# Kernel optimization log

Hardware: AMD Instinct MI355X
Metric: run time of the kernel (lower is better)

The kernel has to match this reference:

```python
import jax, jax.numpy as jnp
import numpy as np

D_MODEL, N_HEADS, D_LATENT = 1024, 16, 256
HEAD_DIM = D_MODEL // N_HEADS
B, T = 2, 2048


def apply_rope(x):
    # x: [B, T, H, D]
    Tn, D = x.shape[1], x.shape[3]
    inv_freq = 1.0 / (10000.0 ** (jnp.arange(0, D, 2, dtype=jnp.float32) / D))
    t = jnp.arange(Tn, dtype=jnp.float32)
    freqs = jnp.outer(t, inv_freq)               # [T, D/2]
    sin_f = jnp.sin(freqs)[None, :, None, :]
    cos_f = jnp.cos(freqs)[None, :, None, :]
    x1, x2 = jnp.split(x, 2, axis=-1)
    return jnp.concatenate([x1 * cos_f - x2 * sin_f,
                            x1 * sin_f + x2 * cos_f], axis=-1)


def setup_inputs() -> dict:
    key = jax.random.key(0)
    ks = jax.random.split(key, 5)
    s = lambda fan_in: 1.0 / np.sqrt(fan_in)
    return {
        "x": jax.random.normal(ks[0], (B, T, D_MODEL), jnp.float32),
        "Wq": jax.random.normal(ks[1], (D_MODEL, D_MODEL), jnp.float32) * s(D_MODEL),
        "bq": jnp.zeros((D_MODEL,), jnp.float32),
        "Wkv_down": jax.random.normal(ks[2], (D_MODEL, D_LATENT), jnp.float32) * s(D_MODEL),
        "bkv_down": jnp.zeros((D_LATENT,), jnp.float32),
        "Wkv_up": jax.random.normal(ks[3], (D_LATENT, 2 * D_MODEL), jnp.float32) * s(D_LATENT),
        "bkv_up": jnp.zeros((2 * D_MODEL,), jnp.float32),
        "Wo": jax.random.normal(ks[4], (D_MODEL, D_MODEL), jnp.float32) * s(D_MODEL),
        "bo": jnp.zeros((D_MODEL,), jnp.float32),
    }


def reference(x, Wq, bq, Wkv_down, bkv_down, Wkv_up, bkv_up, Wo, bo):
    Bn, Tn = x.shape[0], x.shape[1]
    q = x @ Wq + bq                              # [B, T, d_model]
    kv = (x @ Wkv_down + bkv_down) @ Wkv_up + bkv_up  # [B, T, 2*d_model]
    q = q.reshape(Bn, Tn, N_HEADS, HEAD_DIM)
    kv = kv.reshape(Bn, Tn, N_HEADS, 2 * HEAD_DIM)
    k, v = jnp.split(kv, 2, axis=-1)
    q = apply_rope(q)
    k = apply_rope(k)
    q = q.transpose(0, 2, 1, 3)                  # [B, H, T, D]
    k = k.transpose(0, 2, 1, 3)
    v = v.transpose(0, 2, 1, 3)

    att = jnp.einsum('bhqd,bhkd->bhqk', q, k) / jnp.sqrt(jnp.float32(HEAD_DIM))

    idx = jnp.arange(Tn, dtype=jnp.float32)
    dist_signed = idx[:, None] - idx[None, :]    # [T, T]
    log_sparse = -0.1 * jnp.log(jnp.abs(dist_signed) + 1.0)
    decay = jnp.exp(-jnp.maximum(dist_signed, 0.0) * 0.01)
    att = att + (log_sparse + jnp.log(decay + 1e-9))[None, None]
    att = jax.nn.softmax(att, axis=-1)
    out = jnp.einsum('bhqk,bhkd->bhqd', att, v)  # [B, H, T, D]

    # Infini/memory branch: mean-pooled single-slot attention
    memory_k = jnp.mean(k, axis=2, keepdims=True)  # [B, H, 1, D]
    memory_v = jnp.mean(v, axis=2, keepdims=True)
    memory_scores = jnp.einsum('bhqd,bhkd->bhqk', q, memory_k)  # [B, H, T, 1]
    infini_out = jax.nn.sigmoid(memory_scores) * memory_v       # [B, H, T, D]
    out = out + 0.2 * infini_out

    out = out.transpose(0, 2, 1, 3).reshape(Bn, Tn, D_MODEL)
    return out @ Wo + bo
```

## Files before the change

kernel.cpp:

```cpp
#include <hip/hip_runtime.h>
#include <hip/hip_bf16.h>

#define D_MODEL 1024
#define N_HEADS 16
#define HEAD_DIM 64
#define D_LATENT 256
#define BATCH 2
#define SEQ 2048
#define M_ROWS (BATCH * SEQ)

typedef __bf16 bf16;
typedef __attribute__((ext_vector_type(4))) __bf16 bf16x4;
typedef __attribute__((ext_vector_type(8))) __bf16 bf16x8;
typedef __attribute__((ext_vector_type(4))) float f32x4;

#define MFMA_BF16(a, b, c) __builtin_amdgcn_mfma_f32_16x16x32_bf16((a), (b), (c), 0, 0, 0)
#define LOG2E 1.4426950408889634f

__device__ __forceinline__ void gll16(const void* g, void* l) {
    __builtin_amdgcn_global_load_lds(
        (const __attribute__((address_space(1))) unsigned int*)g,
        (__attribute__((address_space(3))) unsigned int*)l, 16, 0, 0);
}

__device__ __forceinline__ void tw_body(
    const float* __restrict__ W, bf16* __restrict__ Wt, int K, int N,
    int b, float (*tw)[33], int tid)
{
    int nx = N / 32;
    int n0 = (b % nx) * 32, k0 = (b / nx) * 32;
    int c = tid & 31, r = tid >> 5;
    #pragma unroll
    for (int it = 0; it < 4; ++it)
        tw[r + it * 8][c] = W[(size_t)(k0 + r + it * 8) * N + n0 + c];
    __syncthreads();
    #pragma unroll
    for (int it = 0; it < 4; ++it)
        Wt[(size_t)(n0 + r + it * 8) * K + k0 + c] = (bf16)tw[c][r + it * 8];
}

__global__ __launch_bounds__(256) void prep_all(
    const float* __restrict__ x, bf16* __restrict__ xb,
    const float* __restrict__ Wq, bf16* __restrict__ Wqt,
    const float* __restrict__ Wd, bf16* __restrict__ Wdt,
    const float* __restrict__ Wu, bf16* __restrict__ Wut,
    const float* __restrict__ Wo, bf16* __restrict__ Wot,
    float2* __restrict__ rtab, float* __restrict__ bias2)
{
    __shared__ float tw[32][33];
    const int bid = blockIdx.x, tid = threadIdx.x;
    if (bid < 2048) {
        int i = bid * 256 + tid;
        const float4* s = ((const float4*)x) + (size_t)i * 2;
        float4 a = s[0], b = s[1];
        bf16x8 v;
        v[0] = (bf16)a.x; v[1] = (bf16)a.y; v[2] = (bf16)a.z; v[3] = (bf16)a.w;
        v[4] = (bf16)b.x; v[5] = (bf16)b.y; v[6] = (bf16)b.z; v[7] = (bf16)b.w;
        *(bf16x8*)(xb + (size_t)i * 8) = v;
    } else if (bid < 3072) {
        tw_body(Wq, Wqt, 1024, 1024, bid - 2048, tw, tid);
    } else if (bid < 3328) {
        tw_body(Wd, Wdt, 1024, 256, bid - 3072, tw, tid);
    } else if (bid < 3840) {
        tw_body(Wu, Wut, 256, 2048, bid - 3328, tw, tid);
    } else if (bid < 4864) {
        tw_body(Wo, Wot, 1024, 1024, bid - 3840, tw, tid);
    } else if (bid < 5120) {
        int i = (bid - 4864) * 256 + tid;
        int j = i & 31, t = i >> 5;
        float inv_freq = exp2f((float)j * -0.4152410118609203f);
        float ang = (float)t * inv_freq;
        float sn, cs; sincosf(ang, &sn, &cs);
        rtab[i] = make_float2(cs, sn);
    } else {
        int i = (bid - 5120) * 256 + tid;
        if (i < 2 * SEQ - 1) {
            float d = (float)(i - (SEQ - 1));
            float ls  = -0.1f * logf(fabsf(d) + 1.0f);
            float dec = expf(-fmaxf(d, 0.0f) * 0.01f);
            bias2[i] = (ls + logf(dec + 1e-9f)) * LOG2E;
        }
    }
}

__device__ __forceinline__ void gemm_body(
    const bf16* __restrict__ A, const bf16* __restrict__ Bt, int K,
    bf16* As, bf16* Bs, f32x4 (&acc)[4][4],
    int m0, int n0, int tid, int l15, int lh, int wr, int wc)
{
    for (int k0 = 0; k0 < K; k0 += 32) {
        __syncthreads();
        #pragma unroll
        for (int it = 0; it < 2; ++it) {
            int c = it * 256 + tid;
            int row = c >> 2, part = c & 3;
            int p = part ^ ((row >> 1) & 3);
            gll16(A  + (size_t)(m0 + row) * K + k0 + p * 8, As + c * 8);
            gll16(Bt + (size_t)(n0 + row) * K + k0 + p * 8, Bs + c * 8);
        }
        __syncthreads();
        bf16x8 af[4], bg[4];
        #pragma unroll
        for (int i = 0; i < 4; ++i) {
            int row = wr * 64 + i * 16 + l15;
            int cc = lh ^ ((row >> 1) & 3);
            af[i] = *(const bf16x8*)(As + row * 32 + cc * 8);
        }
        #pragma unroll
        for (int j = 0; j < 4; ++j) {
            int row = wc * 64 + j * 16 + l15;
            int cc = lh ^ ((row >> 1) & 3);
            bg[j] = *(const bf16x8*)(Bs + row * 32 + cc * 8);
        }
        #pragma unroll
        for (int i = 0; i < 4; ++i)
            #pragma unroll
            for (int j = 0; j < 4; ++j)
                acc[i][j] = MFMA_BF16(af[i], bg[j], acc[i][j]);
    }
}

template<int OUT_BF16>
__global__ __launch_bounds__(256) void gemm_plain(
    const bf16* __restrict__ A, const bf16* __restrict__ Bt,
    const float* __restrict__ bias, void* __restrict__ C,
    int N, int K)
{
    __shared__ bf16 As[128 * 32];
    __shared__ bf16 Bs[128 * 32];
    const int tid = threadIdx.x, lane = tid & 63, w = tid >> 6;
    const int wr = w >> 1, wc = w & 1;
    const int l15 = lane & 15, lh = lane >> 4;
    const int m0 = blockIdx.y * 128, n0 = blockIdx.x * 128;
    f32x4 acc[4][4] = {};
    gemm_body(A, Bt, K, As, Bs, acc, m0, n0, tid, l15, lh, wr, wc);

    #pragma unroll
    for (int i = 0; i < 4; ++i) {
        int row = m0 + wr * 64 + i * 16 + lh * 4;
        #pragma unroll
        for (int j = 0; j < 4; ++j) {
            int col = n0 + wc * 64 + j * 16 + l15;
            float bv = bias[col];
            #pragma unroll
            for (int r = 0; r < 4; ++r) {
                float v = acc[i][j][r] + bv;
                if (OUT_BF16) ((bf16*)C)[(size_t)(row + r) * N + col] = (bf16)v;
                else          ((float*)C)[(size_t)(row + r) * N + col] = v;
            }
        }
    }
}

__global__ __launch_bounds__(256) void gemm_q_rope(
    const bf16* __restrict__ A, const bf16* __restrict__ Bt,
    const float* __restrict__ bias, const float2* __restrict__ rtab,
    bf16* __restrict__ Qh)
{
    __shared__ bf16 As[128 * 32];
    __shared__ bf16 Bs[128 * 32];
    const int tid = threadIdx.x, lane = tid & 63, w = tid >> 6;
    const int wr = w >> 1, wc = w & 1;
    const int l15 = lane & 15, lh = lane >> 4;
    const int m0 = blockIdx.y * 128, n0 = blockIdx.x * 128;
    f32x4 acc[4][4] = {};
    gemm_body(A, Bt, D_MODEL, As, Bs, acc, m0, n0, tid, l15, lh, wr, wc);

    const int head = blockIdx.x * 2 + wc;
    #pragma unroll
    for (int i = 0; i < 4; ++i) {
        #pragma unroll
        for (int r = 0; r < 4; ++r) {
            int m = m0 + wr * 64 + i * 16 + lh * 4 + r;
            int tpos = m & (SEQ - 1), b = m >> 11;
            bf16* orow = Qh + ((size_t)(b * N_HEADS + head) * SEQ + tpos) * 64;
            #pragma unroll
            for (int j01 = 0; j01 < 2; ++j01) {
                int jj = j01 * 16 + l15;
                float2 cssn = rtab[tpos * 32 + jj];
                float v1 = acc[i][j01][r]     + bias[head * 64 + jj];
                float v2 = acc[i][j01 + 2][r] + bias[head * 64 + jj + 32];
                orow[jj]      = (bf16)(v1 * cssn.x - v2 * cssn.y);
                orow[jj + 32] = (bf16)(v1 * cssn.y + v2 * cssn.x);
            }
        }
    }
}

__global__ __launch_bounds__(256) void gemm_kv_rope(
    const bf16* __restrict__ A, const bf16* __restrict__ Bt,
    const float* __restrict__ bias, const float2* __restrict__ rtab,
    bf16* __restrict__ Kh, bf16* __restrict__ Vh)
{
    __shared__ bf16 As[128 * 32];
    __shared__ bf16 Bs[128 * 32];
    const int tid = threadIdx.x, lane = tid & 63, w = tid >> 6;
    const int wr = w >> 1, wc = w & 1;
    const int l15 = lane & 15, lh = lane >> 4;
    const int m0 = blockIdx.y * 128, n0 = blockIdx.x * 128;
    f32x4 acc[4][4] = {};
    gemm_body(A, Bt, D_LATENT, As, Bs, acc, m0, n0, tid, l15, lh, wr, wc);

    const int head = blockIdx.x;
    if (wc == 0) {
        #pragma unroll
        for (int i = 0; i < 4; ++i) {
            #pragma unroll
            for (int r = 0; r < 4; ++r) {
                int m = m0 + wr * 64 + i * 16 + lh * 4 + r;
                int tpos = m & (SEQ - 1), b = m >> 11;
                bf16* orow = Kh + ((size_t)(b * N_HEADS + head) * SEQ + tpos) * 64;
                #pragma unroll
                for (int j01 = 0; j01 < 2; ++j01) {
                    int jj = j01 * 16 + l15;
                    float2 cssn = rtab[tpos * 32 + jj];
                    float v1 = acc[i][j01][r]     + bias[head * 128 + jj];
                    float v2 = acc[i][j01 + 2][r] + bias[head * 128 + jj + 32];
                    orow[jj]      = (bf16)(v1 * cssn.x - v2 * cssn.y);
                    orow[jj + 32] = (bf16)(v1 * cssn.y + v2 * cssn.x);
                }
            }
        }
    } else {
        #pragma unroll
        for (int i = 0; i < 4; ++i) {
            #pragma unroll
            for (int r = 0; r < 4; ++r) {
                int m = m0 + wr * 64 + i * 16 + lh * 4 + r;
                int tpos = m & (SEQ - 1), b = m >> 11;
                bf16* orow = Vh + ((size_t)(b * N_HEADS + head) * SEQ + tpos) * 64;
                #pragma unroll
                for (int j = 0; j < 4; ++j) {
                    int d = j * 16 + l15;
                    orow[d] = (bf16)(acc[i][j][r] + bias[head * 128 + 64 + d]);
                }
            }
        }
    }
}

__global__ __launch_bounds__(256) void transpose_v_b(
    const bf16* __restrict__ Vh, bf16* __restrict__ Vt)
{
    __shared__ bf16 tile[64][72];
    int blk = blockIdx.x;
    int tt = blk & 31, bh = blk >> 5;
    int t0 = tt * 64;
    int tid = threadIdx.x;
    #pragma unroll
    for (int it = 0; it < 2; ++it) {
        int lin = it * 256 + tid;
        int r = lin >> 3, c8 = (lin & 7) * 8;
        bf16x8 v = *(const bf16x8*)(Vh + ((size_t)bh * SEQ + t0 + r) * 64 + c8);
        #pragma unroll
        for (int e = 0; e < 8; ++e) tile[c8 + e][r] = v[e];
    }
    __syncthreads();
    #pragma unroll
    for (int it = 0; it < 2; ++it) {
        int lin = it * 256 + tid;
        int d = lin >> 3, seg = (lin & 7) * 8;
        bf16x8 v = *(const bf16x8*)(&tile[d][seg]);
        *(bf16x8*)(Vt + ((size_t)bh * 64 + d) * SEQ + t0 + seg) = v;
    }
}

__global__ __launch_bounds__(256) void mean_part(
    const bf16* __restrict__ Kh, const bf16* __restrict__ Vh,
    float* __restrict__ part)
{
    __shared__ float red[4][128];
    const int bh = blockIdx.x >> 3, seg = blockIdx.x & 7;
    const int tid = threadIdx.x;
    const int rr = tid >> 4, l16 = tid & 15;
    float ak[4] = {}, av[4] = {};
    #pragma unroll 4
    for (int i = 0; i < 16; ++i) {
        int row = seg * 256 + i * 16 + rr;
        const bf16* kp = Kh + ((size_t)bh * SEQ + row) * 64 + l16 * 4;
        const bf16* vp = Vh + ((size_t)bh * SEQ + row) * 64 + l16 * 4;
        bf16x4 k4 = *(const bf16x4*)kp;
        bf16x4 v4 = *(const bf16x4*)vp;
        #pragma unroll
        for (int e = 0; e < 4; ++e) { ak[e] += (float)k4[e]; av[e] += (float)v4[e]; }
    }
    #pragma unroll
    for (int m = 16; m <= 32; m <<= 1)
        #pragma unroll
        for (int e = 0; e < 4; ++e) {
            ak[e] += __shfl_xor(ak[e], m, 64);
            av[e] += __shfl_xor(av[e], m, 64);
        }
    int wv = tid >> 6;
    if ((tid & 63) < 16) {
        #pragma unroll
        for (int e = 0; e < 4; ++e) {
            red[wv][l16 * 4 + e]      = ak[e];
            red[wv][64 + l16 * 4 + e] = av[e];
        }
    }
    __syncthreads();
    if (tid < 128) {
        float s = red[0][tid] + red[1][tid] + red[2][tid] + red[3][tid];
        part[((size_t)seg * 32 + bh) * 128 + tid] = s;
    }
}

__global__ void mean_final(const float* __restrict__ part, float* __restrict__ memkv)
{
    int idx = blockIdx.x * 256 + threadIdx.x;
    float s = 0.f;
    #pragma unroll
    for (int g = 0; g < 8; ++g) s += part[(size_t)g * 4096 + idx];
    memkv[idx] = s * (1.f / SEQ);
}

__global__ __launch_bounds__(256) void attn_mfma(
    const bf16* __restrict__ Qh,
    const bf16* __restrict__ Kh,
    const bf16* __restrict__ Vt,
    const float* __restrict__ bias2,
    const float* __restrict__ memkv,
    bf16* __restrict__ ao)
{
    __shared__ bf16 PQ[4 * 16 * 88];
    __shared__ bf16 Ks[64 * 64];
    __shared__ bf16 Vs[64 * 64];
    __shared__ float bias_s[2112];

    const int tid = threadIdx.x;
    const int lane = tid & 63;
    const int w = tid >> 6;
    const int l15 = lane & 15, lh = lane >> 4;
    const int bh = blockIdx.y;
    const int q0 = blockIdx.x * 64;
    const size_t bhT = (size_t)bh * SEQ;

    for (int i = tid; i < 2111; i += 256) bias_s[i] = bias2[q0 + i];
    #pragma unroll
    for (int it = 0; it < 2; ++it) {
        int c = it * 256 + tid;
        int row = c >> 3, part = c & 7;
        int p = part ^ (row & 7);
        gll16(Qh + (bhT + q0 + row) * 64 + p * 8, PQ + c * 8);
    }
    __syncthreads();

    const int qrow = w * 16 + l15;
    bf16x8 qf[2];
    #pragma unroll
    for (int ks = 0; ks < 2; ++ks) {
        int pp = (ks * 4 + lh) ^ (qrow & 7);
        qf[ks] = *(const bf16x8*)(PQ + qrow * 64 + pp * 8);
    }

    const float* mk = memkv + bh * 128;
    float di = 0.f;
    #pragma unroll
    for (int ks = 0; ks < 2; ++ks)
        #pragma unroll
        for (int e = 0; e < 8; ++e)
            di += (float)qf[ks][e] * mk[ks * 32 + lh * 8 + e];
    di += __shfl_xor(di, 16, 64);
    di += __shfl_xor(di, 32, 64);

    f32x4 o[4] = {};
    float lsum = 0.f;
    bf16* Psw = PQ + w * 16 * 88;

    for (int kt = 0; kt < SEQ / 64; ++kt) {
        __syncthreads();
        #pragma unroll
        for (int it = 0; it < 2; ++it) {
            int c = it * 256 + tid;
            int row = c >> 3, part = c & 7;
            int p = part ^ (row & 7);
            gll16(Kh + (bhT + kt * 64 + row) * 64 + p * 8, Ks + c * 8);
            gll16(Vt + ((size_t)bh * 64 + row) * SEQ + kt * 64 + p * 8, Vs + c * 8);
        }
        __syncthreads();

        f32x4 s_[4] = {};
        #pragma unroll
        for (int ks = 0; ks < 2; ++ks) {
            #pragma unroll
            for (int jk = 0; jk < 4; ++jk) {
                int row = jk * 16 + l15;
                int cc = (ks * 4 + lh) ^ (row & 7);
                bf16x8 kf = *(const bf16x8*)(Ks + row * 64 + cc * 8);
                s_[jk] = MFMA_BF16(kf, qf[ks], s_[jk]);
            }
        }

        #pragma unroll
        for (int jk = 0; jk < 4; ++jk) {
            int idx0 = (w * 16 + l15) - (kt * 64 + jk * 16 + lh * 4) + 2047;
            bf16x4 pb;
            #pragma unroll
            for (int r = 0; r < 4; ++r) {
                float pexp = exp2f(s_[jk][r] * (0.125f * LOG2E) + bias_s[idx0 - r]);
                lsum += pexp;
                pb[r] = (bf16)pexp;
            }
            *(bf16x4*)(Psw + l15 * 88 + jk * 16 + lh * 4) = pb;
        }

        #pragma unroll
        for (int ks = 0; ks < 2; ++ks) {
            bf16x8 pf = *(const bf16x8*)(Psw + l15 * 88 + ks * 32 + lh * 8);
            #pragma unroll
            for (int jd = 0; jd < 4; ++jd) {
                int row = jd * 16 + l15;
                int cc = (ks * 4 + lh) ^ (row & 7);
                bf16x8 vf = *(const bf16x8*)(Vs + row * 64 + cc * 8);
                o[jd] = MFMA_BF16(pf, vf, o[jd]);
            }
        }
    }

    lsum += __shfl_xor(lsum, 16, 64);
    lsum += __shfl_xor(lsum, 32, 64);

    float inv_l[4], sig[4];
    #pragma unroll
    for (int r = 0; r < 4; ++r) {
        int src = lh * 4 + r;
        inv_l[r] = 1.f / __shfl(lsum, src, 64);
        float dd = __shfl(di, src, 64);
        sig[r] = 1.f / (1.f + __expf(-dd));
    }

    const int b = bh >> 4, h = bh & 15;
    #pragma unroll
    for (int jd = 0; jd < 4; ++jd) {
        int d = jd * 16 + l15;
        float mv = mk[64 + d];
        #pragma unroll
        for (int r = 0; r < 4; ++r) {
            int qi = q0 + w * 16 + lh * 4 + r;
            float val = o[jd][r] * inv_l[r] + 0.2f * sig[r] * mv;
            ao[((size_t)(b * SEQ + qi)) * D_MODEL + h * 64 + d] = (bf16)val;
        }
    }
}

extern "C" void kernel_launch(void* const* d_in, const int* in_sizes, int n_in,
                              void* d_out, int out_size, void* d_ws, size_t ws_size,
                              hipStream_t stream)
{
    const float* x        = (const float*)d_in[0];
    const float* Wq       = (const float*)d_in[1];
    const float* bq       = (const float*)d_in[2];
    const float* Wkv_down = (const float*)d_in[3];
    const float* bkv_down = (const float*)d_in[4];
    const float* Wkv_up   = (const float*)d_in[5];
    const float* bkv_up   = (const float*)d_in[6];
    const float* Wo       = (const float*)d_in[7];
    const float* bo       = (const float*)d_in[8];
    float* out = (float*)d_out;

    char* p = (char*)d_ws;
    bf16* xb   = (bf16*)p;  p += 8388608;
    bf16* Wqt  = (bf16*)p;  p += 2097152;
    bf16* Wdt  = (bf16*)p;  p += 524288;
    bf16* Wut  = (bf16*)p;  p += 1048576;
    bf16* Wot  = (bf16*)p;  p += 2097152;
    bf16* kvd  = (bf16*)p;  p += 2097152;
    bf16* Qh   = (bf16*)p;  p += 8388608;
    bf16* Kh   = (bf16*)p;  p += 8388608;
    bf16* Vh   = (bf16*)p;  p += 8388608;
    bf16* Vt   = (bf16*)p;  p += 8388608;
    bf16* ao   = (bf16*)p;  p += 8388608;
    float* memb  = (float*)p; p += 16384;
    float* bias2 = (float*)p; p += 16384;
    float2* rtab = (float2*)p; p += 524288;
    float* partb = (float*)p; p += 131072;

    dim3 blk(256);

    prep_all<<<dim3(5136), blk, 0, stream>>>(
        x, xb, Wq, Wqt, Wkv_down, Wdt, Wkv_up, Wut, Wo, Wot, rtab, bias2);

    gemm_plain<1><<<dim3(D_LATENT / 128, M_ROWS / 128), blk, 0, stream>>>(
        xb, Wdt, bkv_down, kvd, D_LATENT, D_MODEL);
    gemm_q_rope<<<dim3(D_MODEL / 128, M_ROWS / 128), blk, 0, stream>>>(
        xb, Wqt, bq, rtab, Qh);
    gemm_kv_rope<<<dim3(2 * D_MODEL / 128, M_ROWS / 128), blk, 0, stream>>>(
        kvd, Wut, bkv_up, rtab, Kh, Vh);

    transpose_v_b<<<dim3(BATCH * N_HEADS * (SEQ / 64)), blk, 0, stream>>>(Vh, Vt);
    mean_part<<<dim3(BATCH * N_HEADS * 8), blk, 0, stream>>>(Kh, Vh, partb);
    mean_final<<<dim3(16), blk, 0, stream>>>(partb, memb);

    attn_mfma<<<dim3(SEQ / 64, BATCH * N_HEADS), blk, 0, stream>>>(
        Qh, Kh, Vt, bias2, memb, ao);

    gemm_plain<0><<<dim3(D_MODEL / 128, M_ROWS / 128), blk, 0, stream>>>(
        ao, Wot, bo, out, D_MODEL, D_MODEL);
}
```

Baseline: 256.0 us.

## Double-buffer GEMM and attention tiles, fuse Q/KV-down GEMMs and V transpose/mean

GEMM and attention main loops now double-buffer their LDS tiles, prefetching the next K-slice with global_load_lds and waiting on a partial vmcnt before a single barrier. The Q-projection and KV-down GEMMs are merged into one launch. The KV-up GEMM epilogue writes V already transposed through LDS and accumulates the K/V means with atomics into a buffer zeroed in prep. Together these remove the separate transpose and mean kernels, several launches and a global V round trip, at the cost of doubled LDS per block and float atomic ordering nondeterminism in the means.

```diff
diff --git a/kernel.cpp b/kernel.cpp
--- a/kernel.cpp
+++ b/kernel.cpp
@@ -16,12 +16,16 @@
 
 #define MFMA_BF16(a, b, c) __builtin_amdgcn_mfma_f32_16x16x32_bf16((a), (b), (c), 0, 0, 0)
 #define LOG2E 1.4426950408889634f
+#define SBAR() __builtin_amdgcn_s_barrier()
+#define SCHED0() __builtin_amdgcn_sched_barrier(0)
 
 __device__ __forceinline__ void gll16(const void* g, void* l) {
     __builtin_amdgcn_global_load_lds(
         (const __attribute__((address_space(1))) unsigned int*)g,
         (__attribute__((address_space(3))) unsigned int*)l, 16, 0, 0);
 }
+__device__ __forceinline__ void vwait4() { asm volatile("s_waitcnt vmcnt(4)" ::: "memory"); }
+__device__ __forceinline__ void vwait0() { asm volatile("s_waitcnt vmcnt(0)" ::: "memory"); }
 
 __device__ __forceinline__ void tw_body(
     const float* __restrict__ W, bf16* __restrict__ Wt, int K, int N,
@@ -45,7 +49,8 @@
     const float* __restrict__ Wd, bf16* __restrict__ Wdt,
     const float* __restrict__ Wu, bf16* __restrict__ Wut,
     const float* __restrict__ Wo, bf16* __restrict__ Wot,
-    float2* __restrict__ rtab, float* __restrict__ bias2)
+    float2* __restrict__ rtab, float* __restrict__ bias2,
+    float* __restrict__ memb)
 {
     __shared__ float tw[32][33];
     const int bid = blockIdx.x, tid = threadIdx.x;
@@ -80,25 +85,42 @@
             float dec = expf(-fmaxf(d, 0.0f) * 0.01f);
             bias2[i] = (ls + logf(dec + 1e-9f)) * LOG2E;
         }
+        if (i < 4096) memb[i] = 0.f;
+    }
+}
+
+__device__ __forceinline__ void stage_gemm(
+    const bf16* __restrict__ A, const bf16* __restrict__ Bt, int K, int k0,
+    bf16* As, bf16* Bs, int m0, int n0, int tid)
+{
+    #pragma unroll
+    for (int it = 0; it < 2; ++it) {
+        int c = it * 256 + tid;
+        int row = c >> 2, part = c & 3;
+        int p = part ^ ((row >> 1) & 3);
+        gll16(A  + (size_t)(m0 + row) * K + k0 + p * 8, As + c * 8);
+        gll16(Bt + (size_t)(n0 + row) * K + k0 + p * 8, Bs + c * 8);
     }
 }
 
 __device__ __forceinline__ void gemm_body(
     const bf16* __restrict__ A, const bf16* __restrict__ Bt, int K,
-    bf16* As, bf16* Bs, f32x4 (&acc)[4][4],
+    bf16* sh, f32x4 (&acc)[4][4],
     int m0, int n0, int tid, int l15, int lh, int wr, int wc)
 {
+    stage_gemm(A, Bt, K, 0, sh, sh + 8192, m0, n0, tid);
+    int cur = 0;
     for (int k0 = 0; k0 < K; k0 += 32) {
-        __syncthreads();
-        #pragma unroll
-        for (int it = 0; it < 2; ++it) {
-            int c = it * 256 + tid;
-            int row = c >> 2, part = c & 3;
-            int p = part ^ ((row >> 1) & 3);
-            gll16(A  + (size_t)(m0 + row) * K + k0 + p * 8, As + c * 8);
-            gll16(Bt + (size_t)(n0 + row) * K + k0 + p * 8, Bs + c * 8);
-        }
-        __syncthreads();
+        if (k0 + 32 < K) {
+            stage_gemm(A, Bt, K, k0 + 32, sh + (cur ^ 1) * 4096,
+                       sh + 8192 + (cur ^ 1) * 4096, m0, n0, tid);
+            vwait4();
+        } else {
+            vwait0();
+        }
+        SCHED0(); SBAR(); SCHED0();
+        const bf16* As = sh + cur * 4096;
+        const bf16* Bs = sh + 8192 + cur * 4096;
         bf16x8 af[4], bg[4];
         #pragma unroll
         for (int i = 0; i < 4; ++i) {
@@ -117,23 +139,171 @@
             #pragma unroll
             for (int j = 0; j < 4; ++j)
                 acc[i][j] = MFMA_BF16(af[i], bg[j], acc[i][j]);
-    }
-}
-
-template<int OUT_BF16>
-__global__ __launch_bounds__(256) void gemm_plain(
+        SCHED0(); SBAR(); SCHED0();
+        cur ^= 1;
+    }
+}
+
+__global__ __launch_bounds__(256) void gemm_qkvd(
+    const bf16* __restrict__ xb,
+    const bf16* __restrict__ Wqt, const float* __restrict__ bq,
+    const float2* __restrict__ rtab, bf16* __restrict__ Qh,
+    const bf16* __restrict__ Wdt, const float* __restrict__ bkvd,
+    bf16* __restrict__ kvd)
+{
+    __shared__ bf16 sh[16384];
+    const int tid = threadIdx.x, lane = tid & 63, w = tid >> 6;
+    const int wr = w >> 1, wc = w & 1;
+    const int l15 = lane & 15, lh = lane >> 4;
+    const int bx = blockIdx.x;
+    const int m0 = blockIdx.y * 128;
+    const bf16* Bt = (bx < 8) ? Wqt : Wdt;
+    const int n0 = (bx < 8) ? bx * 128 : (bx - 8) * 128;
+
+    f32x4 acc[4][4] = {};
+    gemm_body(xb, Bt, D_MODEL, sh, acc, m0, n0, tid, l15, lh, wr, wc);
+
+    if (bx < 8) {
+        const int head = bx * 2 + wc;
+        #pragma unroll
+        for (int i = 0; i < 4; ++i) {
+            #pragma unroll
+            for (int r = 0; r < 4; ++r) {
+                int m = m0 + wr * 64 + i * 16 + lh * 4 + r;
+                int tpos = m & (SEQ - 1), b = m >> 11;
+                bf16* orow = Qh + ((size_t)(b * N_HEADS + head) * SEQ + tpos) * 64;
+                #pragma unroll
+                for (int j01 = 0; j01 < 2; ++j01) {
+                    int jj = j01 * 16 + l15;
+                    float2 cssn = rtab[tpos * 32 + jj];
+                    float v1 = acc[i][j01][r]     + bq[head * 64 + jj];
+                    float v2 = acc[i][j01 + 2][r] + bq[head * 64 + jj + 32];
+                    orow[jj]      = (bf16)(v1 * cssn.x - v2 * cssn.y);
+                    orow[jj + 32] = (bf16)(v1 * cssn.y + v2 * cssn.x);
+                }
+            }
+        }
+    } else {
+        #pragma unroll
+        for (int i = 0; i < 4; ++i) {
+            int row = m0 + wr * 64 + i * 16 + lh * 4;
+            #pragma unroll
+            for (int j = 0; j < 4; ++j) {
+                int col = n0 + wc * 64 + j * 16 + l15;
+                float bv = bkvd[col];
+                #pragma unroll
+                for (int r = 0; r < 4; ++r)
+                    kvd[(size_t)(row + r) * D_LATENT + col] = (bf16)(acc[i][j][r] + bv);
+            }
+        }
+    }
+}
+
+__global__ __launch_bounds__(256) void gemm_kv_rope(
     const bf16* __restrict__ A, const bf16* __restrict__ Bt,
-    const float* __restrict__ bias, void* __restrict__ C,
-    int N, int K)
-{
-    __shared__ bf16 As[128 * 32];
-    __shared__ bf16 Bs[128 * 32];
+    const float* __restrict__ bias, const float2* __restrict__ rtab,
+    bf16* __restrict__ Kh, bf16* __restrict__ Vt, float* __restrict__ memb)
+{
+    __shared__ bf16 sh[16384];
+    const int tid = threadIdx.x, lane = tid & 63, w = tid >> 6;
+    const int wr = w >> 1, wc = w & 1;
+    const int l15 = lane & 15, lh = lane >> 4;
+    const int head = blockIdx.x;
+    const int m0 = blockIdx.y * 128;
+    const int b = m0 >> 11;
+    const int bh = b * N_HEADS + head;
+    const int tpos0 = m0 & (SEQ - 1);
+
+    f32x4 acc[4][4] = {};
+    gemm_body(A, Bt, D_LATENT, sh, acc, m0, head * 128, tid, l15, lh, wr, wc);
+
+    if (wc == 0) {
+        float s0 = 0.f, s1 = 0.f, s2 = 0.f, s3 = 0.f;
+        #pragma unroll
+        for (int i = 0; i < 4; ++i) {
+            #pragma unroll
+            for (int r = 0; r < 4; ++r) {
+                int m = m0 + wr * 64 + i * 16 + lh * 4 + r;
+                int tpos = m & (SEQ - 1);
+                bf16* orow = Kh + ((size_t)bh * SEQ + tpos) * 64;
+                float2 ca = rtab[tpos * 32 + l15];
+                float v1 = acc[i][0][r] + bias[head * 128 + l15];
+                float v2 = acc[i][2][r] + bias[head * 128 + l15 + 32];
+                float o1 = v1 * ca.x - v2 * ca.y;
+                float o2 = v1 * ca.y + v2 * ca.x;
+                orow[l15]      = (bf16)o1;
+                orow[l15 + 32] = (bf16)o2;
+                float2 cb = rtab[tpos * 32 + 16 + l15];
+                float v3 = acc[i][1][r] + bias[head * 128 + 16 + l15];
+                float v4 = acc[i][3][r] + bias[head * 128 + 48 + l15];
+                float o3 = v3 * cb.x - v4 * cb.y;
+                float o4 = v3 * cb.y + v4 * cb.x;
+                orow[16 + l15] = (bf16)o3;
+                orow[48 + l15] = (bf16)o4;
+                s0 += o1; s1 += o3; s2 += o2; s3 += o4;
+            }
+        }
+        s0 += __shfl_xor(s0, 16, 64); s0 += __shfl_xor(s0, 32, 64);
+        s1 += __shfl_xor(s1, 16, 64); s1 += __shfl_xor(s1, 32, 64);
+        s2 += __shfl_xor(s2, 16, 64); s2 += __shfl_xor(s2, 32, 64);
+        s3 += __shfl_xor(s3, 16, 64); s3 += __shfl_xor(s3, 32, 64);
+        if (lane < 16) {
+            const float sc = 1.f / SEQ;
+            atomicAdd(&memb[bh * 128 + l15],      s0 * sc);
+            atomicAdd(&memb[bh * 128 + 16 + l15], s1 * sc);
+            atomicAdd(&memb[bh * 128 + 32 + l15], s2 * sc);
+            atomicAdd(&memb[bh * 128 + 48 + l15], s3 * sc);
+        }
+    } else {
+        float sv[4] = {};
+        #pragma unroll
+        for (int i = 0; i < 4; ++i) {
+            #pragma unroll
+            for (int j = 0; j < 4; ++j) {
+                int d = j * 16 + l15;
+                float bv = bias[head * 128 + 64 + d];
+                #pragma unroll
+                for (int r = 0; r < 4; ++r) {
+                    int t = wr * 64 + i * 16 + lh * 4 + r;
+                    float v = acc[i][j][r] + bv;
+                    sh[d * 136 + t] = (bf16)v;
+                    sv[j] += v;
+                }
+            }
+        }
+        #pragma unroll
+        for (int j = 0; j < 4; ++j) {
+            sv[j] += __shfl_xor(sv[j], 16, 64);
+            sv[j] += __shfl_xor(sv[j], 32, 64);
+        }
+        if (lane < 16) {
+            const float sc = 1.f / SEQ;
+            #pragma unroll
+            for (int j = 0; j < 4; ++j)
+                atomicAdd(&memb[bh * 128 + 64 + j * 16 + l15], sv[j] * sc);
+        }
+    }
+    __syncthreads();
+    {
+        int d = tid >> 2, seg = tid & 3;
+        bf16* dst = Vt + ((size_t)bh * 64 + d) * SEQ + tpos0 + seg * 32;
+        #pragma unroll
+        for (int e = 0; e < 4; ++e)
+            *(bf16x8*)(dst + e * 8) = *(const bf16x8*)(sh + d * 136 + seg * 32 + e * 8);
+    }
+}
+
+__global__ __launch_bounds__(256) void gemm_out(
+    const bf16* __restrict__ A, const bf16* __restrict__ Bt,
+    const float* __restrict__ bias, float* __restrict__ C)
+{
+    __shared__ bf16 sh[16384];
     const int tid = threadIdx.x, lane = tid & 63, w = tid >> 6;
     const int wr = w >> 1, wc = w & 1;
     const int l15 = lane & 15, lh = lane >> 4;
     const int m0 = blockIdx.y * 128, n0 = blockIdx.x * 128;
     f32x4 acc[4][4] = {};
-    gemm_body(A, Bt, K, As, Bs, acc, m0, n0, tid, l15, lh, wr, wc);
+    gemm_body(A, Bt, D_MODEL, sh, acc, m0, n0, tid, l15, lh, wr, wc);
 
     #pragma unroll
     for (int i = 0; i < 4; ++i) {
@@ -143,176 +313,10 @@
             int col = n0 + wc * 64 + j * 16 + l15;
             float bv = bias[col];
             #pragma unroll
-            for (int r = 0; r < 4; ++r) {
-                float v = acc[i][j][r] + bv;
-                if (OUT_BF16) ((bf16*)C)[(size_t)(row + r) * N + col] = (bf16)v;
-                else          ((float*)C)[(size_t)(row + r) * N + col] = v;
-            }
-        }
-    }
-}
-
-__global__ __launch_bounds__(256) void gemm_q_rope(
-    const bf16* __restrict__ A, const bf16* __restrict__ Bt,
-    const float* __restrict__ bias, const float2* __restrict__ rtab,
-    bf16* __restrict__ Qh)
-{
-    __shared__ bf16 As[128 * 32];
-    __shared__ bf16 Bs[128 * 32];
-    const int tid = threadIdx.x, lane = tid & 63, w = tid >> 6;
-    const int wr = w >> 1, wc = w & 1;
-    const int l15 = lane & 15, lh = lane >> 4;
-    const int m0 = blockIdx.y * 128, n0 = blockIdx.x * 128;
-    f32x4 acc[4][4] = {};
-    gemm_body(A, Bt, D_MODEL, As, Bs, acc, m0, n0, tid, l15, lh, wr, wc);
-
-    const int head = blockIdx.x * 2 + wc;
-    #pragma unroll
-    for (int i = 0; i < 4; ++i) {
-        #pragma unroll
-        for (int r = 0; r < 4; ++r) {
-            int m = m0 + wr * 64 + i * 16 + lh * 4 + r;
-            int tpos = m & (SEQ - 1), b = m >> 11;
-            bf16* orow = Qh + ((size_t)(b * N_HEADS + head) * SEQ + tpos) * 64;
-            #pragma unroll
-            for (int j01 = 0; j01 < 2; ++j01) {
-                int jj = j01 * 16 + l15;
-                float2 cssn = rtab[tpos * 32 + jj];
-                float v1 = acc[i][j01][r]     + bias[head * 64 + jj];
-                float v2 = acc[i][j01 + 2][r] + bias[head * 64 + jj + 32];
-                orow[jj]      = (bf16)(v1 * cssn.x - v2 * cssn.y);
-                orow[jj + 32] = (bf16)(v1 * cssn.y + v2 * cssn.x);
-            }
-        }
-    }
-}
-
-__global__ __launch_bounds__(256) void gemm_kv_rope(
-    const bf16* __restrict__ A, const bf16* __restrict__ Bt,
-    const float* __restrict__ bias, const float2* __restrict__ rtab,
-    bf16* __restrict__ Kh, bf16* __restrict__ Vh)
-{
-    __shared__ bf16 As[128 * 32];
-    __shared__ bf16 Bs[128 * 32];
-    const int tid = threadIdx.x, lane = tid & 63, w = tid >> 6;
-    const int wr = w >> 1, wc = w & 1;
-    const int l15 = lane & 15, lh = lane >> 4;
-    const int m0 = blockIdx.y * 128, n0 = blockIdx.x * 128;
-    f32x4 acc[4][4] = {};
-    gemm_body(A, Bt, D_LATENT, As, Bs, acc, m0, n0, tid, l15, lh, wr, wc);
-
-    const int head = blockIdx.x;
-    if (wc == 0) {
-        #pragma unroll
-        for (int i = 0; i < 4; ++i) {
-            #pragma unroll
-            for (int r = 0; r < 4; ++r) {
-                int m = m0 + wr * 64 + i * 16 + lh * 4 + r;
-                int tpos = m & (SEQ - 1), b = m >> 11;
-                bf16* orow = Kh + ((size_t)(b * N_HEADS + head) * SEQ + tpos) * 64;
-                #pragma unroll
-                for (int j01 = 0; j01 < 2; ++j01) {
-                    int jj = j01 * 16 + l15;
-                    float2 cssn = rtab[tpos * 32 + jj];
-                    float v1 = acc[i][j01][r]     + bias[head * 128 + jj];
-                    float v2 = acc[i][j01 + 2][r] + bias[head * 128 + jj + 32];
-                    orow[jj]      = (bf16)(v1 * cssn.x - v2 * cssn.y);
-                    orow[jj + 32] = (bf16)(v1 * cssn.y + v2 * cssn.x);
-                }
-            }
-        }
-    } else {
-        #pragma unroll
-        for (int i = 0; i < 4; ++i) {
-            #pragma unroll
-            for (int r = 0; r < 4; ++r) {
-                int m = m0 + wr * 64 + i * 16 + lh * 4 + r;
-                int tpos = m & (SEQ - 1), b = m >> 11;
-                bf16* orow = Vh + ((size_t)(b * N_HEADS + head) * SEQ + tpos) * 64;
-                #pragma unroll
-                for (int j = 0; j < 4; ++j) {
-                    int d = j * 16 + l15;
-                    orow[d] = (bf16)(acc[i][j][r] + bias[head * 128 + 64 + d]);
-                }
-            }
-        }
-    }
-}
-
-__global__ __launch_bounds__(256) void transpose_v_b(
-    const bf16* __restrict__ Vh, bf16* __restrict__ Vt)
-{
-    __shared__ bf16 tile[64][72];
-    int blk = blockIdx.x;
-    int tt = blk & 31, bh = blk >> 5;
-    int t0 = tt * 64;
-    int tid = threadIdx.x;
-    #pragma unroll
-    for (int it = 0; it < 2; ++it) {
-        int lin = it * 256 + tid;
-        int r = lin >> 3, c8 = (lin & 7) * 8;
-        bf16x8 v = *(const bf16x8*)(Vh + ((size_t)bh * SEQ + t0 + r) * 64 + c8);
-        #pragma unroll
-        for (int e = 0; e < 8; ++e) tile[c8 + e][r] = v[e];
-    }
-    __syncthreads();
-    #pragma unroll
-    for (int it = 0; it < 2; ++it) {
-        int lin = it * 256 + tid;
-        int d = lin >> 3, seg = (lin & 7) * 8;
-        bf16x8 v = *(const bf16x8*)(&tile[d][seg]);
-        *(bf16x8*)(Vt + ((size_t)bh * 64 + d) * SEQ + t0 + seg) = v;
-    }
-}
-
-__global__ __launch_bounds__(256) void mean_part(
-    const bf16* __restrict__ Kh, const bf16* __restrict__ Vh,
-    float* __restrict__ part)
-{
-    __shared__ float red[4][128];
-    const int bh = blockIdx.x >> 3, seg = blockIdx.x & 7;
-    const int tid = threadIdx.x;
-    const int rr = tid >> 4, l16 = tid & 15;
-    float ak[4] = {}, av[4] = {};
-    #pragma unroll 4
-    for (int i = 0; i < 16; ++i) {
-        int row = seg * 256 + i * 16 + rr;
-        const bf16* kp = Kh + ((size_t)bh * SEQ + row) * 64 + l16 * 4;
-        const bf16* vp = Vh + ((size_t)bh * SEQ + row) * 64 + l16 * 4;
-        bf16x4 k4 = *(const bf16x4*)kp;
-        bf16x4 v4 = *(const bf16x4*)vp;
-        #pragma unroll
-        for (int e = 0; e < 4; ++e) { ak[e] += (float)k4[e]; av[e] += (float)v4[e]; }
-    }
-    #pragma unroll
-    for (int m = 16; m <= 32; m <<= 1)
-        #pragma unroll
-        for (int e = 0; e < 4; ++e) {
-            ak[e] += __shfl_xor(ak[e], m, 64);
-            av[e] += __shfl_xor(av[e], m, 64);
-        }
-    int wv = tid >> 6;
-    if ((tid & 63) < 16) {
-        #pragma unroll
-        for (int e = 0; e < 4; ++e) {
-            red[wv][l16 * 4 + e]      = ak[e];
-            red[wv][64 + l16 * 4 + e] = av[e];
-        }
-    }
-    __syncthreads();
-    if (tid < 128) {
-        float s = red[0][tid] + red[1][tid] + red[2][tid] + red[3][tid];
-        part[((size_t)seg * 32 + bh) * 128 + tid] = s;
-    }
-}
-
-__global__ void mean_final(const float* __restrict__ part, float* __restrict__ memkv)
-{
-    int idx = blockIdx.x * 256 + threadIdx.x;
-    float s = 0.f;
-    #pragma unroll
-    for (int g = 0; g < 8; ++g) s += part[(size_t)g * 4096 + idx];
-    memkv[idx] = s * (1.f / SEQ);
+            for (int r = 0; r < 4; ++r)
+                C[(size_t)(row + r) * D_MODEL + col] = acc[i][j][r] + bv;
+        }
+    }
 }
 
 __global__ __launch_bounds__(256) void attn_mfma(
@@ -324,8 +328,8 @@
     bf16* __restrict__ ao)
 {
     __shared__ bf16 PQ[4 * 16 * 88];
-    __shared__ bf16 Ks[64 * 64];
-    __shared__ bf16 Vs[64 * 64];
+    __shared__ bf16 Ks[2 * 64 * 64];
+    __shared__ bf16 Vs[2 * 64 * 64];
     __shared__ float bias_s[2112];
 
     const int tid = threadIdx.x;
@@ -344,6 +348,14 @@
         int p = part ^ (row & 7);
         gll16(Qh + (bhT + q0 + row) * 64 + p * 8, PQ + c * 8);
     }
+    #pragma unroll
+    for (int it = 0; it < 2; ++it) {
+        int c = it * 256 + tid;
+        int row = c >> 3, part = c & 7;
+        int p = part ^ (row & 7);
+        gll16(Kh + (bhT + row) * 64 + p * 8, Ks + c * 8);
+        gll16(Vt + ((size_t)bh * 64 + row) * SEQ + p * 8, Vs + c * 8);
+    }
     __syncthreads();
 
     const int qrow = w * 16 + l15;
@@ -367,18 +379,27 @@
     f32x4 o[4] = {};
     float lsum = 0.f;
     bf16* Psw = PQ + w * 16 * 88;
+    int cur = 0;
 
     for (int kt = 0; kt < SEQ / 64; ++kt) {
-        __syncthreads();
-        #pragma unroll
-        for (int it = 0; it < 2; ++it) {
-            int c = it * 256 + tid;
-            int row = c >> 3, part = c & 7;
-            int p = part ^ (row & 7);
-            gll16(Kh + (bhT + kt * 64 + row) * 64 + p * 8, Ks + c * 8);
-            gll16(Vt + ((size_t)bh * 64 + row) * SEQ + kt * 64 + p * 8, Vs + c * 8);
-        }
-        __syncthreads();
+        if (kt < SEQ / 64 - 1) {
+            #pragma unroll
+            for (int it = 0; it < 2; ++it) {
+                int c = it * 256 + tid;
+                int row = c >> 3, part = c & 7;
+                int p = part ^ (row & 7);
+                gll16(Kh + (bhT + (kt + 1) * 64 + row) * 64 + p * 8,
+                      Ks + (cur ^ 1) * 4096 + c * 8);
+                gll16(Vt + ((size_t)bh * 64 + row) * SEQ + (kt + 1) * 64 + p * 8,
+                      Vs + (cur ^ 1) * 4096 + c * 8);
+            }
+            vwait4();
+        } else {
+            vwait0();
+        }
+        SCHED0(); SBAR(); SCHED0();
+        const bf16* Kc = Ks + cur * 4096;
+        const bf16* Vc = Vs + cur * 4096;
 
         f32x4 s_[4] = {};
         #pragma unroll
@@ -387,7 +408,7 @@
             for (int jk = 0; jk < 4; ++jk) {
                 int row = jk * 16 + l15;
                 int cc = (ks * 4 + lh) ^ (row & 7);
-                bf16x8 kf = *(const bf16x8*)(Ks + row * 64 + cc * 8);
+                bf16x8 kf = *(const bf16x8*)(Kc + row * 64 + cc * 8);
                 s_[jk] = MFMA_BF16(kf, qf[ks], s_[jk]);
             }
         }
@@ -412,10 +433,12 @@
             for (int jd = 0; jd < 4; ++jd) {
                 int row = jd * 16 + l15;
                 int cc = (ks * 4 + lh) ^ (row & 7);
-                bf16x8 vf = *(const bf16x8*)(Vs + row * 64 + cc * 8);
+                bf16x8 vf = *(const bf16x8*)(Vc + row * 64 + cc * 8);
                 o[jd] = MFMA_BF16(pf, vf, o[jd]);
             }
         }
+        SCHED0(); SBAR(); SCHED0();
+        cur ^= 1;
     }
 
     lsum += __shfl_xor(lsum, 16, 64);
@@ -468,33 +491,26 @@
     bf16* kvd  = (bf16*)p;  p += 2097152;
     bf16* Qh   = (bf16*)p;  p += 8388608;
     bf16* Kh   = (bf16*)p;  p += 8388608;
-    bf16* Vh   = (bf16*)p;  p += 8388608;
     bf16* Vt   = (bf16*)p;  p += 8388608;
     bf16* ao   = (bf16*)p;  p += 8388608;
     float* memb  = (float*)p; p += 16384;
     float* bias2 = (float*)p; p += 16384;
     float2* rtab = (float2*)p; p += 524288;
-    float* partb = (float*)p; p += 131072;
 
     dim3 blk(256);
 
     prep_all<<<dim3(5136), blk, 0, stream>>>(
-        x, xb, Wq, Wqt, Wkv_down, Wdt, Wkv_up, Wut, Wo, Wot, rtab, bias2);
-
-    gemm_plain<1><<<dim3(D_LATENT / 128, M_ROWS / 128), blk, 0, stream>>>(
-        xb, Wdt, bkv_down, kvd, D_LATENT, D_MODEL);
-    gemm_q_rope<<<dim3(D_MODEL / 128, M_ROWS / 128), blk, 0, stream>>>(
-        xb, Wqt, bq, rtab, Qh);
-    gemm_kv_rope<<<dim3(2 * D_MODEL / 128, M_ROWS / 128), blk, 0, stream>>>(
-        kvd, Wut, bkv_up, rtab, Kh, Vh);
-
-    transpose_v_b<<<dim3(BATCH * N_HEADS * (SEQ / 64)), blk, 0, stream>>>(Vh, Vt);
-    mean_part<<<dim3(BATCH * N_HEADS * 8), blk, 0, stream>>>(Kh, Vh, partb);
-    mean_final<<<dim3(16), blk, 0, stream>>>(partb, memb);
+        x, xb, Wq, Wqt, Wkv_down, Wdt, Wkv_up, Wut, Wo, Wot, rtab, bias2, memb);
+
+    gemm_qkvd<<<dim3(10, M_ROWS / 128), blk, 0, stream>>>(
+        xb, Wqt, bq, rtab, Qh, Wdt, bkv_down, kvd);
+
+    gemm_kv_rope<<<dim3(N_HEADS, M_ROWS / 128), blk, 0, stream>>>(
+        kvd, Wut, bkv_up, rtab, Kh, Vt, memb);
 
     attn_mfma<<<dim3(SEQ / 64, BATCH * N_HEADS), blk, 0, stream>>>(
         Qh, Kh, Vt, bias2, memb, ao);
 
-    gemm_plain<0><<<dim3(D_MODEL / 128, M_ROWS / 128), blk, 0, stream>>>(
-        ao, Wot, bo, out, D_MODEL, D_MODEL);
-}
+    gemm_out<<<dim3(D_MODEL / 128, M_ROWS / 128), blk, 0, stream>>>(
+        ao, Wot, bo, out);
+}
```

Measured after the change: 223.0 us. 12.9% less time.
